# Optimization experiments

Hardware: AMD Instinct MI355X
Metric: run time of the kernel (lower is better)

## Reference

```python
import jax, jax.numpy as jnp
import numpy as np

B, S, D, KC = 32, 4096, 64, 256  # batch*heads, seq_len, head_dim, compressed dim


def setup_inputs() -> dict:
    key = jax.random.key(0)
    ks = jax.random.split(key, 7)
    return {
        "Q": jax.random.normal(ks[0], (B, S, D), dtype=jnp.float32),
        "K": jax.random.normal(ks[1], (B, S, D), dtype=jnp.float32),
        "V": jax.random.normal(ks[2], (B, S, D), dtype=jnp.float32),
        "E_w": jax.random.normal(ks[3], (KC, S), dtype=jnp.float32) * (1.0 / np.sqrt(S)),
        "E_b": jax.random.normal(ks[4], (KC,), dtype=jnp.float32) * 0.01,
        "F_w": jax.random.normal(ks[5], (KC, S), dtype=jnp.float32) * (1.0 / np.sqrt(S)),
        "F_b": jax.random.normal(ks[6], (KC,), dtype=jnp.float32) * 0.01,
    }


def reference(Q, K, V, E_w, E_b, F_w, F_b):
    # K: [B,S,D] -> transpose -> [B,D,S]; E proj over seq axis -> [B,D,KC]
    Ke = jnp.einsum("bsd,ks->bdk", K, E_w) + E_b  # [B, D, KC]
    # scores: Q @ E(K) -> [B, S, KC], scaled by sqrt(head_dim)
    scale = jnp.sqrt(jnp.asarray(D, dtype=Q.dtype))
    P = jnp.einsum("bsd,bdk->bsk", Q, Ke) / scale
    # causal mask: torch.triu(ones(S, KC)) keeps (i, j) where j >= i
    i = jnp.arange(S)[:, None]
    j = jnp.arange(KC)[None, :]
    keep = j >= i  # [S, KC]
    P = jnp.where(keep[None, :, :], P, jnp.asarray(-1e10, dtype=P.dtype))
    P = jax.nn.softmax(P, axis=-1)  # dropout p=0.0 -> identity
    # V: [B,S,D] -> [B,D,S]; F proj -> [B,D,KC]; transpose -> [B,KC,D]
    Vf = jnp.einsum("bsd,ks->bkd", V, F_w) + F_b[None, :, None]  # [B, KC, D]
    out = jnp.einsum("bsk,bkd->bsd", P, Vf)  # [B, S, D]
    return out
```

## Files before the change

### kernel.cpp

```cpp
#include <hip/hip_runtime.h>
#include <hip/hip_bf16.h>
#include <math.h>

#define NB  32
#define NS  4096
#define ND  64
#define NKC 256

#define BK   128
#define KHALF 2048
#define ASA  132
#define ASB  132

#define QSTR  72
#define PBSTR 264
#define VSTR  264

typedef __attribute__((ext_vector_type(8))) short short8;
typedef __attribute__((ext_vector_type(4))) float f32x4;

__device__ __forceinline__ short f2bf(float f) {
    union { float f; unsigned u; } v; v.f = f;
    return (short)((v.u + 0x7FFFu + ((v.u >> 16) & 1u)) >> 16);
}

__global__ __launch_bounds__(256) void prep(
    const float* __restrict__ Ew, const float* __restrict__ Fw,
    short* __restrict__ EwB, short* __restrict__ FwB)
{
    const int gid = blockIdx.x * 256 + threadIdx.x;
    const int half = (NKC * NS) / 8;
    const float* src = (gid < half) ? Ew : Fw;
    short* dst       = (gid < half) ? EwB : FwB;
    const int i8 = (gid < half) ? gid : gid - half;
    float4 a = *(const float4*)&src[(size_t)i8 * 8];
    float4 c = *(const float4*)&src[(size_t)i8 * 8 + 4];
    short8 w;
    w[0] = f2bf(a.x); w[1] = f2bf(a.y); w[2] = f2bf(a.z); w[3] = f2bf(a.w);
    w[4] = f2bf(c.x); w[5] = f2bf(c.y); w[6] = f2bf(c.z); w[7] = f2bf(c.w);
    *(short8*)&dst[(size_t)i8 * 8] = w;
}

template <typename AT>
__global__ __launch_bounds__(256, 2) void proj_sk(
    const AT* __restrict__ EwX, const AT* __restrict__ FwX,
    const float* __restrict__ K, const float* __restrict__ V,
    float* __restrict__ KeTa, float* __restrict__ Vfa,
    float* __restrict__ KeTb, float* __restrict__ Vfb)
{
    const int bid = blockIdx.x;
    const int r8 = bid & 7, mt = (bid >> 3) & 3, gq = bid >> 5;
    const int grp = gq * 8 + r8;
    const int kh = grp & 1, mm = (grp >> 1) & 1, b = grp >> 2;

    const AT* __restrict__ Ab    = mm ? FwX : EwX;
    const float* __restrict__ Bg = mm ? V   : K;
    float* __restrict__ Cout = kh ? (mm ? Vfb : KeTb) : (mm ? Vfa : KeTa);

    const int t = threadIdx.x, wave = t >> 6, lane = t & 63;
    const int lm = lane & 15, g4 = lane >> 4;
    __shared__ short As[64 * ASA];
    __shared__ short Bs[64 * ASB];
    const size_t bBase = (size_t)b * NS * ND;
    const size_t aBase = (size_t)mt * 64 * NS;
    const int rA = t >> 4, jA = t & 15;
    const int dB = t & 31, sB = t >> 5;

    f32x4 acc[4];
#pragma unroll
    for (int nt = 0; nt < 4; ++nt) acc[nt] = (f32x4){0.f, 0.f, 0.f, 0.f};

    short8 pa[4];
    float4 paf[8];
    float2 pb[16];

    const int sBeg = kh * KHALF, sEnd = sBeg + KHALF;

#pragma unroll
    for (int i = 0; i < 4; ++i) {
        if constexpr (sizeof(AT) == 2) {
            pa[i] = *(const short8*)&Ab[aBase + (size_t)(i * 16 + rA) * NS + sBeg + jA * 8];
        } else {
            paf[2 * i]     = *(const float4*)&Ab[aBase + (size_t)(i * 16 + rA) * NS + sBeg + jA * 8];
            paf[2 * i + 1] = *(const float4*)&Ab[aBase + (size_t)(i * 16 + rA) * NS + sBeg + jA * 8 + 4];
        }
    }
#pragma unroll
    for (int h = 0; h < 2; ++h)
#pragma unroll
        for (int i = 0; i < 8; ++i)
            pb[h * 8 + i] = *(const float2*)&Bg[bBase + (size_t)(sBeg + h * 64 + sB * 8 + i) * ND + dB * 2];

    for (int s0 = sBeg; s0 < sEnd; s0 += BK) {
#pragma unroll
        for (int i = 0; i < 4; ++i) {
            if constexpr (sizeof(AT) == 2) {
                *(short8*)&As[(i * 16 + rA) * ASA + jA * 8] = pa[i];
            } else {
                short8 w;
                w[0] = f2bf(paf[2 * i].x);     w[1] = f2bf(paf[2 * i].y);
                w[2] = f2bf(paf[2 * i].z);     w[3] = f2bf(paf[2 * i].w);
                w[4] = f2bf(paf[2 * i + 1].x); w[5] = f2bf(paf[2 * i + 1].y);
                w[6] = f2bf(paf[2 * i + 1].z); w[7] = f2bf(paf[2 * i + 1].w);
                *(short8*)&As[(i * 16 + rA) * ASA + jA * 8] = w;
            }
        }
#pragma unroll
        for (int h = 0; h < 2; ++h) {
            short8 w0, w1;
#pragma unroll
            for (int i = 0; i < 8; ++i) {
                w0[i] = f2bf(pb[h * 8 + i].x);
                w1[i] = f2bf(pb[h * 8 + i].y);
            }
            *(short8*)&Bs[(dB * 2 + 0) * ASB + h * 64 + sB * 8] = w0;
            *(short8*)&Bs[(dB * 2 + 1) * ASB + h * 64 + sB * 8] = w1;
        }
        __syncthreads();

        if (s0 + BK < sEnd) {
            const int sn = s0 + BK;
#pragma unroll
            for (int i = 0; i < 4; ++i) {
                if constexpr (sizeof(AT) == 2) {
                    pa[i] = *(const short8*)&Ab[aBase + (size_t)(i * 16 + rA) * NS + sn + jA * 8];
                } else {
                    paf[2 * i]     = *(const float4*)&Ab[aBase + (size_t)(i * 16 + rA) * NS + sn + jA * 8];
                    paf[2 * i + 1] = *(const float4*)&Ab[aBase + (size_t)(i * 16 + rA) * NS + sn + jA * 8 + 4];
                }
            }
#pragma unroll
            for (int h = 0; h < 2; ++h)
#pragma unroll
                for (int i = 0; i < 8; ++i)
                    pb[h * 8 + i] = *(const float2*)&Bg[bBase + (size_t)(sn + h * 64 + sB * 8 + i) * ND + dB * 2];
        }

#pragma unroll
        for (int ks = 0; ks < BK; ks += 32) {
            short8 aF = *(const short8*)&As[(wave * 16 + lm) * ASA + ks + g4 * 8];
#pragma unroll
            for (int nt = 0; nt < 4; ++nt) {
                short8 bF = *(const short8*)&Bs[(nt * 16 + lm) * ASB + ks + g4 * 8];
                acc[nt] = __builtin_amdgcn_mfma_f32_16x16x32_bf16(aF, bF, acc[nt], 0, 0, 0);
            }
        }
        __syncthreads();
    }

#pragma unroll
    for (int nt = 0; nt < 4; ++nt)
#pragma unroll
        for (int rr = 0; rr < 4; ++rr) {
            int kc = mt * 64 + wave * 16 + g4 * 4 + rr;
            Cout[((size_t)b * NKC + kc) * ND + nt * 16 + lm] = acc[nt][rr];
        }
}

__global__ __launch_bounds__(256) void reduce2(
    float4* __restrict__ Areg, const float4* __restrict__ Breg)
{
    const int gid = blockIdx.x * 256 + threadIdx.x;
    float4 a = Areg[gid], c = Breg[gid];
    Areg[gid] = (float4){a.x + c.x, a.y + c.y, a.z + c.z, a.w + c.w};
}

__global__ __launch_bounds__(256) void attn_fused(
    const float* __restrict__ Q,  const float* __restrict__ KeT,
    const float* __restrict__ Vf, const float* __restrict__ Eb,
    const float* __restrict__ Fb, float* __restrict__ out)
{
    const int x = blockIdx.x, b = blockIdx.y, t = threadIdx.x;

    if (x >= 8) {
        __shared__ float pq[16][64];
        __shared__ float mv[64];
        const int kg = t >> 4, dq = t & 15;
        float4 s4 = (float4){0.f, 0.f, 0.f, 0.f};
        for (int p = 0; p < 16; ++p) {
            int k = p * 16 + kg;
            float4 v = *(const float4*)&Vf[((size_t)b * NKC + k) * ND + dq * 4];
            float fb = Fb[k];
            s4.x += v.x + fb; s4.y += v.y + fb; s4.z += v.z + fb; s4.w += v.w + fb;
        }
        *(float4*)&pq[kg][dq * 4] = s4;
        __syncthreads();
        if (t < 64) {
            float m = 0.f;
#pragma unroll
            for (int i = 0; i < 16; ++i) m += pq[i][t];
            mv[t] = m * (1.f / 256.f);
        }
        __syncthreads();
        const int r0 = 256 + (x - 8) * 64;
#pragma unroll
        for (int i = 0; i < 4; ++i) {
            int idx = i * 256 + t, row = idx >> 4, q = idx & 15;
            *(float4*)&out[((size_t)b * NS + r0 + row) * ND + q * 4] =
                *(const float4*)&mv[q * 4];
        }
        return;
    }

    const int s0 = x * 32;
    const int wave = t >> 6, lane = t & 63, lm = lane & 15, g = lane >> 4;
    __shared__ short Qs[32 * QSTR];
    __shared__ short PsB[32 * PBSTR];
    __shared__ short VfT[64 * VSTR];
    __shared__ float rsums[32][4];

    {
        int row = t >> 3, dq = t & 7;
        size_t off = ((size_t)b * NS + s0 + row) * ND + dq * 8;
        float4 q0 = *(const float4*)&Q[off], q1 = *(const float4*)&Q[off + 4];
        short8 w;
        w[0] = f2bf(q0.x); w[1] = f2bf(q0.y); w[2] = f2bf(q0.z); w[3] = f2bf(q0.w);
        w[4] = f2bf(q1.x); w[5] = f2bf(q1.y); w[6] = f2bf(q1.z); w[7] = f2bf(q1.w);
        *(short8*)&Qs[row * QSTR + dq * 8] = w;
    }
    {
        const int dB = t & 31, sB = t >> 5;
#pragma unroll
        for (int pass = 0; pass < 4; ++pass) {
            int kb = pass * 64 + sB * 8;
            float2 v[8]; float fb[8];
#pragma unroll
            for (int i = 0; i < 8; ++i) {
                v[i]  = *(const float2*)&Vf[((size_t)b * NKC + kb + i) * ND + dB * 2];
                fb[i] = Fb[kb + i];
            }
            short8 w0, w1;
#pragma unroll
            for (int i = 0; i < 8; ++i) {
                w0[i] = f2bf(v[i].x + fb[i]);
                w1[i] = f2bf(v[i].y + fb[i]);
            }
            *(short8*)&VfT[(dB * 2 + 0) * VSTR + kb] = w0;
            *(short8*)&VfT[(dB * 2 + 1) * VSTR + kb] = w1;
        }
    }
    __syncthreads();

    f32x4 accP[2][4];
#pragma unroll
    for (int rt = 0; rt < 2; ++rt)
#pragma unroll
        for (int kk = 0; kk < 4; ++kk) accP[rt][kk] = (f32x4){0.f, 0.f, 0.f, 0.f};
#pragma unroll
    for (int kk = 0; kk < 4; ++kk) {
        int kt = wave * 4 + kk;
        float ebv = Eb[kt * 16 + lm];
#pragma unroll
        for (int ks2 = 0; ks2 < 2; ++ks2) {
            const float* kp = &KeT[((size_t)b * NKC + kt * 16 + lm) * ND + ks2 * 32 + g * 8];
            float4 c0 = *(const float4*)kp, c1 = *(const float4*)(kp + 4);
            short8 bf;
            bf[0] = f2bf(c0.x + ebv); bf[1] = f2bf(c0.y + ebv);
            bf[2] = f2bf(c0.z + ebv); bf[3] = f2bf(c0.w + ebv);
            bf[4] = f2bf(c1.x + ebv); bf[5] = f2bf(c1.y + ebv);
            bf[6] = f2bf(c1.z + ebv); bf[7] = f2bf(c1.w + ebv);
#pragma unroll
            for (int rt = 0; rt < 2; ++rt) {
                short8 aq = *(const short8*)&Qs[(rt * 16 + lm) * QSTR + ks2 * 32 + g * 8];
                accP[rt][kk] = __builtin_amdgcn_mfma_f32_16x16x32_bf16(aq, bf, accP[rt][kk], 0, 0, 0);
            }
        }
    }
#pragma unroll
    for (int rt = 0; rt < 2; ++rt)
#pragma unroll
        for (int r = 0; r < 4; ++r) {
            float s = 0.f;
            int rowg = s0 + rt * 16 + g * 4 + r;
#pragma unroll
            for (int kk = 0; kk < 4; ++kk) {
                int col = wave * 64 + kk * 16 + lm;
                float e = (col >= rowg) ? __expf(accP[rt][kk][r] * 0.125f) : 0.f;
                accP[rt][kk][r] = e;
                s += e;
            }
#pragma unroll
            for (int off = 1; off <= 8; off <<= 1) s += __shfl_xor(s, off, 64);
            if (lm == 0) rsums[rt * 16 + g * 4 + r][wave] = s;
        }
    __syncthreads();
#pragma unroll
    for (int rt = 0; rt < 2; ++rt)
#pragma unroll
        for (int r = 0; r < 4; ++r) {
            float4 rs = *(const float4*)&rsums[rt * 16 + g * 4 + r][0];
            float inv = 1.f / (rs.x + rs.y + rs.z + rs.w);
#pragma unroll
            for (int kk = 0; kk < 4; ++kk)
                PsB[(rt * 16 + g * 4 + r) * PBSTR + wave * 64 + kk * 16 + lm] =
                    f2bf(accP[rt][kk][r] * inv);
        }
    __syncthreads();

    f32x4 oa[2];
    oa[0] = (f32x4){0.f, 0.f, 0.f, 0.f};
    oa[1] = (f32x4){0.f, 0.f, 0.f, 0.f};
    for (int ks = x; ks < 8; ++ks) {
        short8 bv = *(const short8*)&VfT[(wave * 16 + lm) * VSTR + ks * 32 + g * 8];
#pragma unroll
        for (int rt = 0; rt < 2; ++rt) {
            short8 av = *(const short8*)&PsB[(rt * 16 + lm) * PBSTR + ks * 32 + g * 8];
            oa[rt] = __builtin_amdgcn_mfma_f32_16x16x32_bf16(av, bv, oa[rt], 0, 0, 0);
        }
    }
#pragma unroll
    for (int rt = 0; rt < 2; ++rt)
#pragma unroll
        for (int r = 0; r < 4; ++r)
            out[((size_t)b * NS + s0 + rt * 16 + g * 4 + r) * ND + wave * 16 + lm] = oa[rt][r];
}

extern "C" void kernel_launch(void* const* d_in, const int* in_sizes, int n_in,
                              void* d_out, int out_size, void* d_ws, size_t ws_size,
                              hipStream_t stream) {
    (void)in_sizes; (void)n_in; (void)out_size;
    const float* Q  = (const float*)d_in[0];
    const float* K  = (const float*)d_in[1];
    const float* V  = (const float*)d_in[2];
    const float* Ew = (const float*)d_in[3];
    const float* Eb = (const float*)d_in[4];
    const float* Fw = (const float*)d_in[5];
    const float* Fb = (const float*)d_in[6];
    float* out = (float*)d_out;

    const size_t nKe = (size_t)NB * NKC * ND;
    float* base = (float*)d_ws;
    float* KeTa = base;
    float* Vfa  = base + nKe;
    float* KeTb = base + 2 * nKe;
    float* Vfb  = base + 3 * nKe;

    if (ws_size >= 12u * 1024 * 1024) {
        short* EwB = (short*)(base + 4 * nKe);
        short* FwB = EwB + (size_t)NKC * NS;
        prep<<<dim3(1024), 256, 0, stream>>>(Ew, Fw, EwB, FwB);
        proj_sk<short><<<dim3(512), 256, 0, stream>>>(EwB, FwB, K, V,
                                                      KeTa, Vfa, KeTb, Vfb);
    } else {
        proj_sk<float><<<dim3(512), 256, 0, stream>>>(Ew, Fw, K, V,
                                                      KeTa, Vfa, KeTb, Vfb);
    }
    reduce2<<<dim3(1024), 256, 0, stream>>>((float4*)base,
                                            (const float4*)(base + 2 * nKe));
    attn_fused<<<dim3(68, NB), 256, 0, stream>>>(Q, KeTa, Vfa, Eb, Fb, out);
}
```

Before: 185.6 us.

## Double-buffer projection LDS, drop prep and reduce kernels, fold split-K sum

The projection kernel now uses two LDS buffers with a software pipeline, so the bf16 conversion and staging of the next K tile overlaps the MFMA work on the current one, and B-operand registers are double-buffered as well. The separate prep kernel that converted E/F weights to bf16 is removed, and weights are converted inline from fp32. The reduce2 kernel is also removed, and the attention kernel sums the two split-K halves itself when it loads them. This cuts two launches and their memory round trips, at the cost of more LDS and registers in proj_sk and extra global reads of both halves in attn_fused.

```diff
diff --git a/kernel.cpp b/kernel.cpp
--- a/kernel.cpp
+++ b/kernel.cpp
@@ -7,10 +7,11 @@
 #define ND  64
 #define NKC 256
 
-#define BK   128
+#define BK    128
 #define KHALF 2048
-#define ASA  132
-#define ASB  132
+#define NIT   16
+#define ASA   132
+#define ASB   132
 
 #define QSTR  72
 #define PBSTR 264
@@ -24,26 +25,8 @@
     return (short)((v.u + 0x7FFFu + ((v.u >> 16) & 1u)) >> 16);
 }
 
-__global__ __launch_bounds__(256) void prep(
+__global__ __launch_bounds__(256, 2) void proj_sk(
     const float* __restrict__ Ew, const float* __restrict__ Fw,
-    short* __restrict__ EwB, short* __restrict__ FwB)
-{
-    const int gid = blockIdx.x * 256 + threadIdx.x;
-    const int half = (NKC * NS) / 8;
-    const float* src = (gid < half) ? Ew : Fw;
-    short* dst       = (gid < half) ? EwB : FwB;
-    const int i8 = (gid < half) ? gid : gid - half;
-    float4 a = *(const float4*)&src[(size_t)i8 * 8];
-    float4 c = *(const float4*)&src[(size_t)i8 * 8 + 4];
-    short8 w;
-    w[0] = f2bf(a.x); w[1] = f2bf(a.y); w[2] = f2bf(a.z); w[3] = f2bf(a.w);
-    w[4] = f2bf(c.x); w[5] = f2bf(c.y); w[6] = f2bf(c.z); w[7] = f2bf(c.w);
-    *(short8*)&dst[(size_t)i8 * 8] = w;
-}
-
-template <typename AT>
-__global__ __launch_bounds__(256, 2) void proj_sk(
-    const AT* __restrict__ EwX, const AT* __restrict__ FwX,
     const float* __restrict__ K, const float* __restrict__ V,
     float* __restrict__ KeTa, float* __restrict__ Vfa,
     float* __restrict__ KeTb, float* __restrict__ Vfb)
@@ -53,14 +36,14 @@
     const int grp = gq * 8 + r8;
     const int kh = grp & 1, mm = (grp >> 1) & 1, b = grp >> 2;
 
-    const AT* __restrict__ Ab    = mm ? FwX : EwX;
-    const float* __restrict__ Bg = mm ? V   : K;
+    const float* __restrict__ Ab = mm ? Fw : Ew;
+    const float* __restrict__ Bg = mm ? V  : K;
     float* __restrict__ Cout = kh ? (mm ? Vfb : KeTb) : (mm ? Vfa : KeTa);
 
     const int t = threadIdx.x, wave = t >> 6, lane = t & 63;
     const int lm = lane & 15, g4 = lane >> 4;
-    __shared__ short As[64 * ASA];
-    __shared__ short Bs[64 * ASB];
+    __shared__ short As[2][64 * ASA];
+    __shared__ short Bs[2][64 * ASB];
     const size_t bBase = (size_t)b * NS * ND;
     const size_t aBase = (size_t)mt * 64 * NS;
     const int rA = t >> 4, jA = t & 15;
@@ -70,40 +53,34 @@
 #pragma unroll
     for (int nt = 0; nt < 4; ++nt) acc[nt] = (f32x4){0.f, 0.f, 0.f, 0.f};
 
-    short8 pa[4];
     float4 paf[8];
-    float2 pb[16];
-
-    const int sBeg = kh * KHALF, sEnd = sBeg + KHALF;
-
-#pragma unroll
-    for (int i = 0; i < 4; ++i) {
-        if constexpr (sizeof(AT) == 2) {
-            pa[i] = *(const short8*)&Ab[aBase + (size_t)(i * 16 + rA) * NS + sBeg + jA * 8];
-        } else {
-            paf[2 * i]     = *(const float4*)&Ab[aBase + (size_t)(i * 16 + rA) * NS + sBeg + jA * 8];
-            paf[2 * i + 1] = *(const float4*)&Ab[aBase + (size_t)(i * 16 + rA) * NS + sBeg + jA * 8 + 4];
-        }
-    }
-#pragma unroll
-    for (int h = 0; h < 2; ++h)
-#pragma unroll
-        for (int i = 0; i < 8; ++i)
-            pb[h * 8 + i] = *(const float2*)&Bg[bBase + (size_t)(sBeg + h * 64 + sB * 8 + i) * ND + dB * 2];
-
-    for (int s0 = sBeg; s0 < sEnd; s0 += BK) {
+    float2 pbA[16], pbB[16];
+
+    const int sBeg = kh * KHALF;
+
+    auto loadA = [&](int s) {
 #pragma unroll
         for (int i = 0; i < 4; ++i) {
-            if constexpr (sizeof(AT) == 2) {
-                *(short8*)&As[(i * 16 + rA) * ASA + jA * 8] = pa[i];
-            } else {
-                short8 w;
-                w[0] = f2bf(paf[2 * i].x);     w[1] = f2bf(paf[2 * i].y);
-                w[2] = f2bf(paf[2 * i].z);     w[3] = f2bf(paf[2 * i].w);
-                w[4] = f2bf(paf[2 * i + 1].x); w[5] = f2bf(paf[2 * i + 1].y);
-                w[6] = f2bf(paf[2 * i + 1].z); w[7] = f2bf(paf[2 * i + 1].w);
-                *(short8*)&As[(i * 16 + rA) * ASA + jA * 8] = w;
-            }
+            paf[2 * i]     = *(const float4*)&Ab[aBase + (size_t)(i * 16 + rA) * NS + s + jA * 8];
+            paf[2 * i + 1] = *(const float4*)&Ab[aBase + (size_t)(i * 16 + rA) * NS + s + jA * 8 + 4];
+        }
+    };
+    auto loadB = [&](float2* pb, int s) {
+#pragma unroll
+        for (int h = 0; h < 2; ++h)
+#pragma unroll
+            for (int i = 0; i < 8; ++i)
+                pb[h * 8 + i] = *(const float2*)&Bg[bBase + (size_t)(s + h * 64 + sB * 8 + i) * ND + dB * 2];
+    };
+    auto stage = [&](int buf, const float2* pb) {
+#pragma unroll
+        for (int i = 0; i < 4; ++i) {
+            short8 w;
+            w[0] = f2bf(paf[2 * i].x);     w[1] = f2bf(paf[2 * i].y);
+            w[2] = f2bf(paf[2 * i].z);     w[3] = f2bf(paf[2 * i].w);
+            w[4] = f2bf(paf[2 * i + 1].x); w[5] = f2bf(paf[2 * i + 1].y);
+            w[6] = f2bf(paf[2 * i + 1].z); w[7] = f2bf(paf[2 * i + 1].w);
+            *(short8*)&As[buf][(i * 16 + rA) * ASA + jA * 8] = w;
         }
 #pragma unroll
         for (int h = 0; h < 2; ++h) {
@@ -113,39 +90,44 @@
                 w0[i] = f2bf(pb[h * 8 + i].x);
                 w1[i] = f2bf(pb[h * 8 + i].y);
             }
-            *(short8*)&Bs[(dB * 2 + 0) * ASB + h * 64 + sB * 8] = w0;
-            *(short8*)&Bs[(dB * 2 + 1) * ASB + h * 64 + sB * 8] = w1;
-        }
+            *(short8*)&Bs[buf][(dB * 2 + 0) * ASB + h * 64 + sB * 8] = w0;
+            *(short8*)&Bs[buf][(dB * 2 + 1) * ASB + h * 64 + sB * 8] = w1;
+        }
+    };
+    auto domfma = [&](int buf) {
+#pragma unroll
+        for (int ks = 0; ks < BK; ks += 32) {
+            short8 aF = *(const short8*)&As[buf][(wave * 16 + lm) * ASA + ks + g4 * 8];
+#pragma unroll
+            for (int nt = 0; nt < 4; ++nt) {
+                short8 bF = *(const short8*)&Bs[buf][(nt * 16 + lm) * ASB + ks + g4 * 8];
+                acc[nt] = __builtin_amdgcn_mfma_f32_16x16x32_bf16(aF, bF, acc[nt], 0, 0, 0);
+            }
+        }
+    };
+
+    loadA(sBeg);
+    loadB(pbA, sBeg);
+    stage(0, pbA);
+    loadA(sBeg + BK);
+    loadB(pbA, sBeg + BK);
+    loadB(pbB, sBeg + 2 * BK);
+    __syncthreads();
+
+    for (int ip = 0; ip < NIT / 2; ++ip) {
+        const int i0 = 2 * ip;
+        domfma(0);
+        stage(1, pbA);
+        if (i0 + 3 < NIT) loadB(pbA, sBeg + (i0 + 3) * BK);
+        if (i0 + 2 < NIT) loadA(sBeg + (i0 + 2) * BK);
         __syncthreads();
-
-        if (s0 + BK < sEnd) {
-            const int sn = s0 + BK;
-#pragma unroll
-            for (int i = 0; i < 4; ++i) {
-                if constexpr (sizeof(AT) == 2) {
-                    pa[i] = *(const short8*)&Ab[aBase + (size_t)(i * 16 + rA) * NS + sn + jA * 8];
-                } else {
-                    paf[2 * i]     = *(const float4*)&Ab[aBase + (size_t)(i * 16 + rA) * NS + sn + jA * 8];
-                    paf[2 * i + 1] = *(const float4*)&Ab[aBase + (size_t)(i * 16 + rA) * NS + sn + jA * 8 + 4];
-                }
-            }
-#pragma unroll
-            for (int h = 0; h < 2; ++h)
-#pragma unroll
-                for (int i = 0; i < 8; ++i)
-                    pb[h * 8 + i] = *(const float2*)&Bg[bBase + (size_t)(sn + h * 64 + sB * 8 + i) * ND + dB * 2];
-        }
-
-#pragma unroll
-        for (int ks = 0; ks < BK; ks += 32) {
-            short8 aF = *(const short8*)&As[(wave * 16 + lm) * ASA + ks + g4 * 8];
-#pragma unroll
-            for (int nt = 0; nt < 4; ++nt) {
-                short8 bF = *(const short8*)&Bs[(nt * 16 + lm) * ASB + ks + g4 * 8];
-                acc[nt] = __builtin_amdgcn_mfma_f32_16x16x32_bf16(aF, bF, acc[nt], 0, 0, 0);
-            }
-        }
-        __syncthreads();
+        domfma(1);
+        if (i0 + 2 < NIT) {
+            stage(0, pbB);
+            if (i0 + 4 < NIT) loadB(pbB, sBeg + (i0 + 4) * BK);
+            if (i0 + 3 < NIT) loadA(sBeg + (i0 + 3) * BK);
+            __syncthreads();
+        }
     }
 
 #pragma unroll
@@ -157,18 +139,12 @@
         }
 }
 
-__global__ __launch_bounds__(256) void reduce2(
-    float4* __restrict__ Areg, const float4* __restrict__ Breg)
-{
-    const int gid = blockIdx.x * 256 + threadIdx.x;
-    float4 a = Areg[gid], c = Breg[gid];
-    Areg[gid] = (float4){a.x + c.x, a.y + c.y, a.z + c.z, a.w + c.w};
-}
-
 __global__ __launch_bounds__(256) void attn_fused(
-    const float* __restrict__ Q,  const float* __restrict__ KeT,
-    const float* __restrict__ Vf, const float* __restrict__ Eb,
-    const float* __restrict__ Fb, float* __restrict__ out)
+    const float* __restrict__ Q,
+    const float* __restrict__ KeTa, const float* __restrict__ Vfa,
+    const float* __restrict__ KeTb, const float* __restrict__ Vfb,
+    const float* __restrict__ Eb,  const float* __restrict__ Fb,
+    float* __restrict__ out)
 {
     const int x = blockIdx.x, b = blockIdx.y, t = threadIdx.x;
 
@@ -179,9 +155,11 @@
         float4 s4 = (float4){0.f, 0.f, 0.f, 0.f};
         for (int p = 0; p < 16; ++p) {
             int k = p * 16 + kg;
-            float4 v = *(const float4*)&Vf[((size_t)b * NKC + k) * ND + dq * 4];
+            float4 v = *(const float4*)&Vfa[((size_t)b * NKC + k) * ND + dq * 4];
+            float4 u = *(const float4*)&Vfb[((size_t)b * NKC + k) * ND + dq * 4];
             float fb = Fb[k];
-            s4.x += v.x + fb; s4.y += v.y + fb; s4.z += v.z + fb; s4.w += v.w + fb;
+            s4.x += (v.x + u.x) + fb; s4.y += (v.y + u.y) + fb;
+            s4.z += (v.z + u.z) + fb; s4.w += (v.w + u.w) + fb;
         }
         *(float4*)&pq[kg][dq * 4] = s4;
         __syncthreads();
@@ -223,17 +201,18 @@
 #pragma unroll
         for (int pass = 0; pass < 4; ++pass) {
             int kb = pass * 64 + sB * 8;
-            float2 v[8]; float fb[8];
+            float2 v[8], u[8]; float fb[8];
 #pragma unroll
             for (int i = 0; i < 8; ++i) {
-                v[i]  = *(const float2*)&Vf[((size_t)b * NKC + kb + i) * ND + dB * 2];
+                v[i]  = *(const float2*)&Vfa[((size_t)b * NKC + kb + i) * ND + dB * 2];
+                u[i]  = *(const float2*)&Vfb[((size_t)b * NKC + kb + i) * ND + dB * 2];
                 fb[i] = Fb[kb + i];
             }
             short8 w0, w1;
 #pragma unroll
             for (int i = 0; i < 8; ++i) {
-                w0[i] = f2bf(v[i].x + fb[i]);
-                w1[i] = f2bf(v[i].y + fb[i]);
+                w0[i] = f2bf((v[i].x + u[i].x) + fb[i]);
+                w1[i] = f2bf((v[i].y + u[i].y) + fb[i]);
             }
             *(short8*)&VfT[(dB * 2 + 0) * VSTR + kb] = w0;
             *(short8*)&VfT[(dB * 2 + 1) * VSTR + kb] = w1;
@@ -252,13 +231,14 @@
         float ebv = Eb[kt * 16 + lm];
 #pragma unroll
         for (int ks2 = 0; ks2 < 2; ++ks2) {
-            const float* kp = &KeT[((size_t)b * NKC + kt * 16 + lm) * ND + ks2 * 32 + g * 8];
-            float4 c0 = *(const float4*)kp, c1 = *(const float4*)(kp + 4);
+            const size_t koff = ((size_t)b * NKC + kt * 16 + lm) * ND + ks2 * 32 + g * 8;
+            float4 c0 = *(const float4*)&KeTa[koff], c1 = *(const float4*)&KeTa[koff + 4];
+            float4 e0 = *(const float4*)&KeTb[koff], e1 = *(const float4*)&KeTb[koff + 4];
             short8 bf;
-            bf[0] = f2bf(c0.x + ebv); bf[1] = f2bf(c0.y + ebv);
-            bf[2] = f2bf(c0.z + ebv); bf[3] = f2bf(c0.w + ebv);
-            bf[4] = f2bf(c1.x + ebv); bf[5] = f2bf(c1.y + ebv);
-            bf[6] = f2bf(c1.z + ebv); bf[7] = f2bf(c1.w + ebv);
+            bf[0] = f2bf((c0.x + e0.x) + ebv); bf[1] = f2bf((c0.y + e0.y) + ebv);
+            bf[2] = f2bf((c0.z + e0.z) + ebv); bf[3] = f2bf((c0.w + e0.w) + ebv);
+            bf[4] = f2bf((c1.x + e1.x) + ebv); bf[5] = f2bf((c1.y + e1.y) + ebv);
+            bf[6] = f2bf((c1.z + e1.z) + ebv); bf[7] = f2bf((c1.w + e1.w) + ebv);
 #pragma unroll
             for (int rt = 0; rt < 2; ++rt) {
                 short8 aq = *(const short8*)&Qs[(rt * 16 + lm) * QSTR + ks2 * 32 + g * 8];
@@ -318,7 +298,7 @@
 extern "C" void kernel_launch(void* const* d_in, const int* in_sizes, int n_in,
                               void* d_out, int out_size, void* d_ws, size_t ws_size,
                               hipStream_t stream) {
-    (void)in_sizes; (void)n_in; (void)out_size;
+    (void)in_sizes; (void)n_in; (void)out_size; (void)ws_size;
     const float* Q  = (const float*)d_in[0];
     const float* K  = (const float*)d_in[1];
     const float* V  = (const float*)d_in[2];
@@ -335,17 +315,7 @@
     float* KeTb = base + 2 * nKe;
     float* Vfb  = base + 3 * nKe;
 
-    if (ws_size >= 12u * 1024 * 1024) {
-        short* EwB = (short*)(base + 4 * nKe);
-        short* FwB = EwB + (size_t)NKC * NS;
-        prep<<<dim3(1024), 256, 0, stream>>>(Ew, Fw, EwB, FwB);
-        proj_sk<short><<<dim3(512), 256, 0, stream>>>(EwB, FwB, K, V,
-                                                      KeTa, Vfa, KeTb, Vfb);
-    } else {
-        proj_sk<float><<<dim3(512), 256, 0, stream>>>(Ew, Fw, K, V,
-                                                      KeTa, Vfa, KeTb, Vfb);
-    }
-    reduce2<<<dim3(1024), 256, 0, stream>>>((float4*)base,
-                                            (const float4*)(base + 2 * nKe));
-    attn_fused<<<dim3(68, NB), 256, 0, stream>>>(Q, KeTa, Vfa, Eb, Fb, out);
+    proj_sk<<<dim3(512), 256, 0, stream>>>(Ew, Fw, K, V, KeTa, Vfa, KeTb, Vfb);
+    attn_fused<<<dim3(68, NB), 256, 0, stream>>>(Q, KeTa, Vfa, KeTb, Vfb,
+                                                 Eb, Fb, out);
 }
```

Result: slower. 194.6 us (+4.8%).

## Fold split-K partial reduction into attention kernel and widen blocks to 512 threads

Applied to the files above, without the earlier changes.

Drops the separate reduce2 kernel that summed the two split-K partial projections. The attention kernel now reads both partial buffers and adds them while loading Ke and Vf. Blocks grow from 256 to 512 threads (8 waves), so each wave handles fewer score columns and a single output tile. This saves one kernel launch and one read-write pass over the workspace, at the cost of every attention block re-reading both partial buffers.

```diff
diff --git a/kernel.cpp b/kernel.cpp
--- a/kernel.cpp
+++ b/kernel.cpp
@@ -7,16 +7,17 @@
 #define ND  64
 #define NKC 256
 
-#define BK   128
+#define BK    128
 #define KHALF 2048
-#define ASA  132
-#define ASB  132
+#define ASA   132
+#define ASB   132
 
 #define QSTR  72
 #define PBSTR 264
 #define VSTR  264
 
 typedef __attribute__((ext_vector_type(8))) short short8;
+typedef __attribute__((ext_vector_type(4))) short short4v;
 typedef __attribute__((ext_vector_type(4))) float f32x4;
 
 __device__ __forceinline__ short f2bf(float f) {
@@ -157,45 +158,42 @@
         }
 }
 
-__global__ __launch_bounds__(256) void reduce2(
-    float4* __restrict__ Areg, const float4* __restrict__ Breg)
-{
-    const int gid = blockIdx.x * 256 + threadIdx.x;
-    float4 a = Areg[gid], c = Breg[gid];
-    Areg[gid] = (float4){a.x + c.x, a.y + c.y, a.z + c.z, a.w + c.w};
-}
-
-__global__ __launch_bounds__(256) void attn_fused(
-    const float* __restrict__ Q,  const float* __restrict__ KeT,
-    const float* __restrict__ Vf, const float* __restrict__ Eb,
-    const float* __restrict__ Fb, float* __restrict__ out)
+__global__ __launch_bounds__(512) void attn_fused(
+    const float* __restrict__ Q,
+    const float* __restrict__ KeTa, const float* __restrict__ Vfa,
+    const float* __restrict__ KeTb, const float* __restrict__ Vfb,
+    const float* __restrict__ Eb,  const float* __restrict__ Fb,
+    float* __restrict__ out)
 {
     const int x = blockIdx.x, b = blockIdx.y, t = threadIdx.x;
 
     if (x >= 8) {
-        __shared__ float pq[16][64];
+        __shared__ float pq[32][64];
         __shared__ float mv[64];
         const int kg = t >> 4, dq = t & 15;
         float4 s4 = (float4){0.f, 0.f, 0.f, 0.f};
-        for (int p = 0; p < 16; ++p) {
-            int k = p * 16 + kg;
-            float4 v = *(const float4*)&Vf[((size_t)b * NKC + k) * ND + dq * 4];
+#pragma unroll
+        for (int p = 0; p < 8; ++p) {
+            int k = p * 32 + kg;
+            float4 v = *(const float4*)&Vfa[((size_t)b * NKC + k) * ND + dq * 4];
+            float4 u = *(const float4*)&Vfb[((size_t)b * NKC + k) * ND + dq * 4];
             float fb = Fb[k];
-            s4.x += v.x + fb; s4.y += v.y + fb; s4.z += v.z + fb; s4.w += v.w + fb;
+            s4.x += (v.x + u.x) + fb; s4.y += (v.y + u.y) + fb;
+            s4.z += (v.z + u.z) + fb; s4.w += (v.w + u.w) + fb;
         }
         *(float4*)&pq[kg][dq * 4] = s4;
         __syncthreads();
         if (t < 64) {
             float m = 0.f;
 #pragma unroll
-            for (int i = 0; i < 16; ++i) m += pq[i][t];
+            for (int i = 0; i < 32; ++i) m += pq[i][t];
             mv[t] = m * (1.f / 256.f);
         }
         __syncthreads();
         const int r0 = 256 + (x - 8) * 64;
 #pragma unroll
-        for (int i = 0; i < 4; ++i) {
-            int idx = i * 256 + t, row = idx >> 4, q = idx & 15;
+        for (int i = 0; i < 2; ++i) {
+            int idx = i * 512 + t, row = idx >> 4, q = idx & 15;
             *(float4*)&out[((size_t)b * NS + r0 + row) * ND + q * 4] =
                 *(const float4*)&mv[q * 4];
         }
@@ -207,33 +205,33 @@
     __shared__ short Qs[32 * QSTR];
     __shared__ short PsB[32 * PBSTR];
     __shared__ short VfT[64 * VSTR];
-    __shared__ float rsums[32][4];
+    __shared__ float rsums[32][8];
 
     {
-        int row = t >> 3, dq = t & 7;
-        size_t off = ((size_t)b * NS + s0 + row) * ND + dq * 8;
-        float4 q0 = *(const float4*)&Q[off], q1 = *(const float4*)&Q[off + 4];
-        short8 w;
+        int row = t >> 4, dq = t & 15;
+        size_t off = ((size_t)b * NS + s0 + row) * ND + dq * 4;
+        float4 q0 = *(const float4*)&Q[off];
+        short4v w;
         w[0] = f2bf(q0.x); w[1] = f2bf(q0.y); w[2] = f2bf(q0.z); w[3] = f2bf(q0.w);
-        w[4] = f2bf(q1.x); w[5] = f2bf(q1.y); w[6] = f2bf(q1.z); w[7] = f2bf(q1.w);
-        *(short8*)&Qs[row * QSTR + dq * 8] = w;
+        *(short4v*)&Qs[row * QSTR + dq * 4] = w;
     }
     {
         const int dB = t & 31, sB = t >> 5;
 #pragma unroll
-        for (int pass = 0; pass < 4; ++pass) {
-            int kb = pass * 64 + sB * 8;
-            float2 v[8]; float fb[8];
+        for (int pass = 0; pass < 2; ++pass) {
+            int kb = pass * 128 + sB * 8;
+            float2 v[8], u[8]; float fb[8];
 #pragma unroll
             for (int i = 0; i < 8; ++i) {
-                v[i]  = *(const float2*)&Vf[((size_t)b * NKC + kb + i) * ND + dB * 2];
+                v[i]  = *(const float2*)&Vfa[((size_t)b * NKC + kb + i) * ND + dB * 2];
+                u[i]  = *(const float2*)&Vfb[((size_t)b * NKC + kb + i) * ND + dB * 2];
                 fb[i] = Fb[kb + i];
             }
             short8 w0, w1;
 #pragma unroll
             for (int i = 0; i < 8; ++i) {
-                w0[i] = f2bf(v[i].x + fb[i]);
-                w1[i] = f2bf(v[i].y + fb[i]);
+                w0[i] = f2bf((v[i].x + u[i].x) + fb[i]);
+                w1[i] = f2bf((v[i].y + u[i].y) + fb[i]);
             }
             *(short8*)&VfT[(dB * 2 + 0) * VSTR + kb] = w0;
             *(short8*)&VfT[(dB * 2 + 1) * VSTR + kb] = w1;
@@ -241,24 +239,25 @@
     }
     __syncthreads();
 
-    f32x4 accP[2][4];
+    f32x4 accP[2][2];
 #pragma unroll
     for (int rt = 0; rt < 2; ++rt)
 #pragma unroll
-        for (int kk = 0; kk < 4; ++kk) accP[rt][kk] = (f32x4){0.f, 0.f, 0.f, 0.f};
-#pragma unroll
-    for (int kk = 0; kk < 4; ++kk) {
-        int kt = wave * 4 + kk;
+        for (int kk = 0; kk < 2; ++kk) accP[rt][kk] = (f32x4){0.f, 0.f, 0.f, 0.f};
+#pragma unroll
+    for (int kk = 0; kk < 2; ++kk) {
+        int kt = wave * 2 + kk;
         float ebv = Eb[kt * 16 + lm];
 #pragma unroll
         for (int ks2 = 0; ks2 < 2; ++ks2) {
-            const float* kp = &KeT[((size_t)b * NKC + kt * 16 + lm) * ND + ks2 * 32 + g * 8];
-            float4 c0 = *(const float4*)kp, c1 = *(const float4*)(kp + 4);
+            const size_t koff = ((size_t)b * NKC + kt * 16 + lm) * ND + ks2 * 32 + g * 8;
+            float4 c0 = *(const float4*)&KeTa[koff], c1 = *(const float4*)&KeTa[koff + 4];
+            float4 e0 = *(const float4*)&KeTb[koff], e1 = *(const float4*)&KeTb[koff + 4];
             short8 bf;
-            bf[0] = f2bf(c0.x + ebv); bf[1] = f2bf(c0.y + ebv);
-            bf[2] = f2bf(c0.z + ebv); bf[3] = f2bf(c0.w + ebv);
-            bf[4] = f2bf(c1.x + ebv); bf[5] = f2bf(c1.y + ebv);
-            bf[6] = f2bf(c1.z + ebv); bf[7] = f2bf(c1.w + ebv);
+            bf[0] = f2bf((c0.x + e0.x) + ebv); bf[1] = f2bf((c0.y + e0.y) + ebv);
+            bf[2] = f2bf((c0.z + e0.z) + ebv); bf[3] = f2bf((c0.w + e0.w) + ebv);
+            bf[4] = f2bf((c1.x + e1.x) + ebv); bf[5] = f2bf((c1.y + e1.y) + ebv);
+            bf[6] = f2bf((c1.z + e1.z) + ebv); bf[7] = f2bf((c1.w + e1.w) + ebv);
 #pragma unroll
             for (int rt = 0; rt < 2; ++rt) {
                 short8 aq = *(const short8*)&Qs[(rt * 16 + lm) * QSTR + ks2 * 32 + g * 8];
@@ -273,8 +272,8 @@
             float s = 0.f;
             int rowg = s0 + rt * 16 + g * 4 + r;
 #pragma unroll
-            for (int kk = 0; kk < 4; ++kk) {
-                int col = wave * 64 + kk * 16 + lm;
+            for (int kk = 0; kk < 2; ++kk) {
+                int col = wave * 32 + kk * 16 + lm;
                 float e = (col >= rowg) ? __expf(accP[rt][kk][r] * 0.125f) : 0.f;
                 accP[rt][kk][r] = e;
                 s += e;
@@ -288,31 +287,27 @@
     for (int rt = 0; rt < 2; ++rt)
 #pragma unroll
         for (int r = 0; r < 4; ++r) {
-            float4 rs = *(const float4*)&rsums[rt * 16 + g * 4 + r][0];
-            float inv = 1.f / (rs.x + rs.y + rs.z + rs.w);
-#pragma unroll
-            for (int kk = 0; kk < 4; ++kk)
-                PsB[(rt * 16 + g * 4 + r) * PBSTR + wave * 64 + kk * 16 + lm] =
+            int row = rt * 16 + g * 4 + r;
+            float4 ra = *(const float4*)&rsums[row][0];
+            float4 rb = *(const float4*)&rsums[row][4];
+            float inv = 1.f / (ra.x + ra.y + ra.z + ra.w + rb.x + rb.y + rb.z + rb.w);
+#pragma unroll
+            for (int kk = 0; kk < 2; ++kk)
+                PsB[row * PBSTR + wave * 32 + kk * 16 + lm] =
                     f2bf(accP[rt][kk][r] * inv);
         }
     __syncthreads();
 
-    f32x4 oa[2];
-    oa[0] = (f32x4){0.f, 0.f, 0.f, 0.f};
-    oa[1] = (f32x4){0.f, 0.f, 0.f, 0.f};
+    const int rt2 = wave >> 2, dt = wave & 3;
+    f32x4 oa = (f32x4){0.f, 0.f, 0.f, 0.f};
     for (int ks = x; ks < 8; ++ks) {
-        short8 bv = *(const short8*)&VfT[(wave * 16 + lm) * VSTR + ks * 32 + g * 8];
-#pragma unroll
-        for (int rt = 0; rt < 2; ++rt) {
-            short8 av = *(const short8*)&PsB[(rt * 16 + lm) * PBSTR + ks * 32 + g * 8];
-            oa[rt] = __builtin_amdgcn_mfma_f32_16x16x32_bf16(av, bv, oa[rt], 0, 0, 0);
-        }
-    }
-#pragma unroll
-    for (int rt = 0; rt < 2; ++rt)
-#pragma unroll
-        for (int r = 0; r < 4; ++r)
-            out[((size_t)b * NS + s0 + rt * 16 + g * 4 + r) * ND + wave * 16 + lm] = oa[rt][r];
+        short8 bv = *(const short8*)&VfT[(dt * 16 + lm) * VSTR + ks * 32 + g * 8];
+        short8 av = *(const short8*)&PsB[(rt2 * 16 + lm) * PBSTR + ks * 32 + g * 8];
+        oa = __builtin_amdgcn_mfma_f32_16x16x32_bf16(av, bv, oa, 0, 0, 0);
+    }
+#pragma unroll
+    for (int r = 0; r < 4; ++r)
+        out[((size_t)b * NS + s0 + rt2 * 16 + g * 4 + r) * ND + dt * 16 + lm] = oa[r];
 }
 
 extern "C" void kernel_launch(void* const* d_in, const int* in_sizes, int n_in,
@@ -345,7 +340,6 @@
         proj_sk<float><<<dim3(512), 256, 0, stream>>>(Ew, Fw, K, V,
                                                       KeTa, Vfa, KeTb, Vfb);
     }
-    reduce2<<<dim3(1024), 256, 0, stream>>>((float4*)base,
-                                            (const float4*)(base + 2 * nKe));
-    attn_fused<<<dim3(68, NB), 256, 0, stream>>>(Q, KeTa, Vfa, Eb, Fb, out);
-}
+    attn_fused<<<dim3(68, NB), 512, 0, stream>>>(Q, KeTa, Vfa, KeTb, Vfb,
+                                                 Eb, Fb, out);
+}
```

After: 189.0 us. About the same (+1.8%).

## Split projection K-dim four ways and fold partial sums into attention

Applied to the files above, without the earlier changes.

The seq-axis split-K of the projection kernel goes from 2 to 4 segments, doubling the grid to 1024 blocks for better CU occupancy. The separate reduce2 kernel is removed: attention blocks sum the partial KeT/Vf slices directly when loading. A small colsum kernel precomputes per-batch column means for the fully masked rows, so the 60 tail blocks per batch just broadcast them. This trades extra partial-buffer reads in attention and more workspace for more projection parallelism and one fewer reduction pass.

```diff
diff --git a/kernel.cpp b/kernel.cpp
--- a/kernel.cpp
+++ b/kernel.cpp
@@ -7,14 +7,15 @@
 #define ND  64
 #define NKC 256
 
-#define BK   128
-#define KHALF 2048
-#define ASA  132
-#define ASB  132
+#define BK    128
+#define ASA   132
+#define ASB   132
 
 #define QSTR  72
 #define PBSTR 264
 #define VSTR  264
+
+#define NKE ((size_t)NB * NKC * ND)
 
 typedef __attribute__((ext_vector_type(8))) short short8;
 typedef __attribute__((ext_vector_type(4))) float f32x4;
@@ -41,21 +42,21 @@
     *(short8*)&dst[(size_t)i8 * 8] = w;
 }
 
-template <typename AT>
-__global__ __launch_bounds__(256, 2) void proj_sk(
+template <typename AT, int NSPL>
+__global__ __launch_bounds__(256, 2 * NSPL / 2) void proj_sk(
     const AT* __restrict__ EwX, const AT* __restrict__ FwX,
     const float* __restrict__ K, const float* __restrict__ V,
-    float* __restrict__ KeTa, float* __restrict__ Vfa,
-    float* __restrict__ KeTb, float* __restrict__ Vfb)
+    float* __restrict__ base)
 {
+    constexpr int KSEG = NS / NSPL;
     const int bid = blockIdx.x;
-    const int r8 = bid & 7, mt = (bid >> 3) & 3, gq = bid >> 5;
-    const int grp = gq * 8 + r8;
-    const int kh = grp & 1, mm = (grp >> 1) & 1, b = grp >> 2;
+    const int r8 = bid & 7, mt = (bid >> 3) & 3, gg = bid >> 5;
+    const int grp = gg * 8 + r8;
+    const int kq = grp % NSPL, mm = (grp / NSPL) & 1, b = grp / (2 * NSPL);
 
     const AT* __restrict__ Ab    = mm ? FwX : EwX;
     const float* __restrict__ Bg = mm ? V   : K;
-    float* __restrict__ Cout = kh ? (mm ? Vfb : KeTb) : (mm ? Vfa : KeTa);
+    float* __restrict__ Cout = base + (size_t)kq * 2 * NKE + (mm ? NKE : 0);
 
     const int t = threadIdx.x, wave = t >> 6, lane = t & 63;
     const int lm = lane & 15, g4 = lane >> 4;
@@ -74,7 +75,7 @@
     float4 paf[8];
     float2 pb[16];
 
-    const int sBeg = kh * KHALF, sEnd = sBeg + KHALF;
+    const int sBeg = kq * KSEG, sEnd = sBeg + KSEG;
 
 #pragma unroll
     for (int i = 0; i < 4; ++i) {
@@ -157,47 +158,83 @@
         }
 }
 
-__global__ __launch_bounds__(256) void reduce2(
-    float4* __restrict__ Areg, const float4* __restrict__ Breg)
+template <int NQ>
+__global__ __launch_bounds__(256) void colsum(
+    const float* __restrict__ base, const float* __restrict__ Fb,
+    float* __restrict__ mv)
 {
-    const int gid = blockIdx.x * 256 + threadIdx.x;
-    float4 a = Areg[gid], c = Breg[gid];
-    Areg[gid] = (float4){a.x + c.x, a.y + c.y, a.z + c.z, a.w + c.w};
-}
-
+    const int b = blockIdx.x, t = threadIdx.x;
+    const int d = t & 63, ks = t >> 6;
+    __shared__ float ps[4][64];
+    __shared__ float fbs[64];
+    float s = 0.f;
+#pragma unroll
+    for (int q = 0; q < NQ; ++q) {
+        const float* Vq = base + (size_t)q * 2 * NKE + NKE + (size_t)b * NKC * ND;
+#pragma unroll 8
+        for (int k = ks * 64; k < ks * 64 + 64; ++k)
+            s += Vq[(size_t)k * ND + d];
+    }
+    ps[ks][d] = s;
+    if (t < 64) fbs[t] = Fb[t] + Fb[t + 64] + Fb[t + 128] + Fb[t + 192];
+    __syncthreads();
+    if (t < 64) {
+        float tot = ps[0][t] + ps[1][t] + ps[2][t] + ps[3][t];
+        float fbsum = 0.f;
+#pragma unroll
+        for (int i = 0; i < 64; ++i) fbsum += fbs[i];
+        mv[(size_t)b * 64 + t] = (tot + fbsum) * (1.f / 256.f);
+    }
+}
+
+template <int NF, bool USEMV>
 __global__ __launch_bounds__(256) void attn_fused(
-    const float* __restrict__ Q,  const float* __restrict__ KeT,
-    const float* __restrict__ Vf, const float* __restrict__ Eb,
+    const float* __restrict__ Q,  const float* __restrict__ base,
+    const float* __restrict__ mv, const float* __restrict__ Eb,
     const float* __restrict__ Fb, float* __restrict__ out)
 {
     const int x = blockIdx.x, b = blockIdx.y, t = threadIdx.x;
 
     if (x >= 8) {
-        __shared__ float pq[16][64];
-        __shared__ float mv[64];
-        const int kg = t >> 4, dq = t & 15;
-        float4 s4 = (float4){0.f, 0.f, 0.f, 0.f};
-        for (int p = 0; p < 16; ++p) {
-            int k = p * 16 + kg;
-            float4 v = *(const float4*)&Vf[((size_t)b * NKC + k) * ND + dq * 4];
-            float fb = Fb[k];
-            s4.x += v.x + fb; s4.y += v.y + fb; s4.z += v.z + fb; s4.w += v.w + fb;
-        }
-        *(float4*)&pq[kg][dq * 4] = s4;
-        __syncthreads();
-        if (t < 64) {
-            float m = 0.f;
-#pragma unroll
-            for (int i = 0; i < 16; ++i) m += pq[i][t];
-            mv[t] = m * (1.f / 256.f);
-        }
-        __syncthreads();
         const int r0 = 256 + (x - 8) * 64;
-#pragma unroll
-        for (int i = 0; i < 4; ++i) {
-            int idx = i * 256 + t, row = idx >> 4, q = idx & 15;
-            *(float4*)&out[((size_t)b * NS + r0 + row) * ND + q * 4] =
-                *(const float4*)&mv[q * 4];
+        if constexpr (USEMV) {
+            float4 val = *(const float4*)&mv[(size_t)b * 64 + (t & 15) * 4];
+            const int rbase = t >> 4;
+#pragma unroll
+            for (int i = 0; i < 4; ++i)
+                *(float4*)&out[((size_t)b * NS + r0 + i * 16 + rbase) * ND + (t & 15) * 4] = val;
+        } else {
+            __shared__ float pq[16][64];
+            __shared__ float mvs[64];
+            const int kg = t >> 4, dq = t & 15;
+            float4 s4 = (float4){0.f, 0.f, 0.f, 0.f};
+            for (int p = 0; p < 16; ++p) {
+                int k = p * 16 + kg;
+                float vx = 0.f, vy = 0.f, vz = 0.f, vw = 0.f;
+#pragma unroll
+                for (int q = 0; q < NF; ++q) {
+                    const float* Vq = base + (size_t)q * 2 * NKE + NKE;
+                    float4 v = *(const float4*)&Vq[((size_t)b * NKC + k) * ND + dq * 4];
+                    vx += v.x; vy += v.y; vz += v.z; vw += v.w;
+                }
+                float fb = Fb[k];
+                s4.x += vx + fb; s4.y += vy + fb; s4.z += vz + fb; s4.w += vw + fb;
+            }
+            *(float4*)&pq[kg][dq * 4] = s4;
+            __syncthreads();
+            if (t < 64) {
+                float m = 0.f;
+#pragma unroll
+                for (int i = 0; i < 16; ++i) m += pq[i][t];
+                mvs[t] = m * (1.f / 256.f);
+            }
+            __syncthreads();
+#pragma unroll
+            for (int i = 0; i < 4; ++i) {
+                int idx = i * 256 + t, row = idx >> 4, q = idx & 15;
+                *(float4*)&out[((size_t)b * NS + r0 + row) * ND + q * 4] =
+                    *(const float4*)&mvs[q * 4];
+            }
         }
         return;
     }
@@ -226,7 +263,14 @@
             float2 v[8]; float fb[8];
 #pragma unroll
             for (int i = 0; i < 8; ++i) {
-                v[i]  = *(const float2*)&Vf[((size_t)b * NKC + kb + i) * ND + dB * 2];
+                float2 s = (float2){0.f, 0.f};
+#pragma unroll
+                for (int q = 0; q < NF; ++q) {
+                    const float* Vq = base + (size_t)q * 2 * NKE + NKE;
+                    float2 xv = *(const float2*)&Vq[((size_t)b * NKC + kb + i) * ND + dB * 2];
+                    s.x += xv.x; s.y += xv.y;
+                }
+                v[i]  = s;
                 fb[i] = Fb[kb + i];
             }
             short8 w0, w1;
@@ -252,8 +296,17 @@
         float ebv = Eb[kt * 16 + lm];
 #pragma unroll
         for (int ks2 = 0; ks2 < 2; ++ks2) {
-            const float* kp = &KeT[((size_t)b * NKC + kt * 16 + lm) * ND + ks2 * 32 + g * 8];
-            float4 c0 = *(const float4*)kp, c1 = *(const float4*)(kp + 4);
+            const size_t koff = ((size_t)b * NKC + kt * 16 + lm) * ND + ks2 * 32 + g * 8;
+            float4 c0 = (float4){0.f, 0.f, 0.f, 0.f};
+            float4 c1 = (float4){0.f, 0.f, 0.f, 0.f};
+#pragma unroll
+            for (int q = 0; q < NF; ++q) {
+                const float* Kq = base + (size_t)q * 2 * NKE;
+                float4 a0 = *(const float4*)&Kq[koff];
+                float4 a1 = *(const float4*)&Kq[koff + 4];
+                c0.x += a0.x; c0.y += a0.y; c0.z += a0.z; c0.w += a0.w;
+                c1.x += a1.x; c1.y += a1.y; c1.z += a1.z; c1.w += a1.w;
+            }
             short8 bf;
             bf[0] = f2bf(c0.x + ebv); bf[1] = f2bf(c0.y + ebv);
             bf[2] = f2bf(c0.z + ebv); bf[3] = f2bf(c0.w + ebv);
@@ -328,24 +381,24 @@
     const float* Fb = (const float*)d_in[6];
     float* out = (float*)d_out;
 
-    const size_t nKe = (size_t)NB * NKC * ND;
     float* base = (float*)d_ws;
-    float* KeTa = base;
-    float* Vfa  = base + nKe;
-    float* KeTb = base + 2 * nKe;
-    float* Vfb  = base + 3 * nKe;
-
-    if (ws_size >= 12u * 1024 * 1024) {
-        short* EwB = (short*)(base + 4 * nKe);
+    const size_t MB = 1024u * 1024u;
+
+    if (ws_size >= 21 * MB) {
+        float* mv  = base + 8 * NKE;
+        short* EwB = (short*)(mv + NB * 64);
         short* FwB = EwB + (size_t)NKC * NS;
         prep<<<dim3(1024), 256, 0, stream>>>(Ew, Fw, EwB, FwB);
-        proj_sk<short><<<dim3(512), 256, 0, stream>>>(EwB, FwB, K, V,
-                                                      KeTa, Vfa, KeTb, Vfb);
+        proj_sk<short, 4><<<dim3(1024), 256, 0, stream>>>(EwB, FwB, K, V, base);
+        colsum<4><<<dim3(NB), 256, 0, stream>>>(base, Fb, mv);
+        attn_fused<4, true><<<dim3(68, NB), 256, 0, stream>>>(Q, base, mv, Eb, Fb, out);
+    } else if (ws_size >= 17 * MB) {
+        float* mv = base + 8 * NKE;
+        proj_sk<float, 4><<<dim3(1024), 256, 0, stream>>>(Ew, Fw, K, V, base);
+        colsum<4><<<dim3(NB), 256, 0, stream>>>(base, Fb, mv);
+        attn_fused<4, true><<<dim3(68, NB), 256, 0, stream>>>(Q, base, mv, Eb, Fb, out);
     } else {
-        proj_sk<float><<<dim3(512), 256, 0, stream>>>(Ew, Fw, K, V,
-                                                      KeTa, Vfa, KeTb, Vfb);
-    }
-    reduce2<<<dim3(1024), 256, 0, stream>>>((float4*)base,
-                                            (const float4*)(base + 2 * nKe));
-    attn_fused<<<dim3(68, NB), 256, 0, stream>>>(Q, KeTa, Vfa, Eb, Fb, out);
-}
+        proj_sk<float, 2><<<dim3(512), 256, 0, stream>>>(Ew, Fw, K, V, base);
+        attn_fused<2, false><<<dim3(68, NB), 256, 0, stream>>>(Q, base, nullptr, Eb, Fb, out);
+    }
+}
```

After: 208.6 us. +12.4%, slower.
